# Kernel optimization log

Hardware: AMD Instinct MI355X
Metric: run time of the kernel (lower is better)

## Reference

```python
import jax, jax.numpy as jnp
import numpy as np


def setup_inputs() -> dict:
    key = jax.random.key(0)
    k1, k2, k3 = jax.random.split(key, 3)
    B, S, D = 4, 2048, 4096
    C, E = 8, 8  # num_clusters, experts per cluster
    hidden_states = jax.random.normal(k1, (B, S, D), dtype=jnp.float32)
    W_cluster = jax.random.normal(k2, (C, D), dtype=jnp.float32) * 0.02
    W_experts = jax.random.normal(k3, (C, E, D), dtype=jnp.float32) * 0.02
    expert_ids = jnp.arange(C * E, dtype=jnp.int64).reshape(C, E)
    return {"hidden_states": hidden_states, "W_cluster": W_cluster,
            "W_experts": W_experts, "expert_ids": expert_ids}


def reference(hidden_states, W_cluster, W_experts, expert_ids):
    # hidden_states: [B, S, D]; W_cluster: [C, D]; W_experts: [C, E, D]; expert_ids: [C, E]
    B, S, D = hidden_states.shape
    C, E, _ = W_experts.shape
    num_total = C * E
    x = hidden_states.reshape(-1, D)                      # [T, D]
    T = x.shape[0]
    # First-level: token-level top-1 cluster routing (cluster_token_routing=True).
    # softmax is monotone, so argmax over logits == argmax over softmax weights.
    cluster_logits = x @ W_cluster.T                      # [T, C]
    cluster_idx = jnp.argmax(cluster_logits, axis=-1)     # [T]
    # Second-level: expert logits for every cluster, then gather the chosen cluster's.
    all_logits = jnp.einsum('td,ced->tce', x, W_experts)  # [T, C, E]
    rows = jnp.arange(T)
    sel_logits = all_logits[rows, cluster_idx]            # [T, E]
    cols = expert_ids[cluster_idx]                        # [T, E] global expert slots
    neg_min = jnp.finfo(hidden_states.dtype).min
    routing = jnp.full((T, num_total), neg_min, dtype=hidden_states.dtype)
    routing = routing.at[rows[:, None], cols].set(sel_logits)
    return routing.reshape(B, S, num_total)
```

## Files before the change

kernel.cpp:

```cpp
#include <hip/hip_runtime.h>
#include <cfloat>

#define DDIM 4096
#define NCLUS 8
#define NEXP 8
#define NOUT 64
#define FILL_BITS 0xFF7F0000u

template <int M>
__device__ __forceinline__ void rs_step(float* a, int lane) {
#pragma unroll
  for (int i = 0; i < M; ++i) {
    float send = (lane & M) ? a[i] : a[i + M];
    float recv = __shfl_xor(send, M, 64);
    a[i] = ((lane & M) ? a[i + M] : a[i]) + recv;
  }
}

__device__ __forceinline__ void reduce32(float* a, int lane) {
#pragma unroll
  for (int i = 0; i < 32; ++i) a[i] += __shfl_xor(a[i], 32, 64);
  rs_step<16>(a, lane);
  rs_step<8>(a, lane);
  rs_step<4>(a, lane);
  rs_step<2>(a, lane);
  rs_step<1>(a, lane);
}

__global__ __launch_bounds__(256) void k_gate(const float* __restrict__ x,
                                              const float* __restrict__ Wc,
                                              const float* __restrict__ We,
                                              const int* __restrict__ eids32,
                                              float* __restrict__ out) {
  const int lane = threadIdx.x & 63;
  const int gw = blockIdx.x * 4 + (threadIdx.x >> 6);
  const int t0 = gw * 4;

  const float* xp = x + (size_t)t0 * DDIM + lane * 4;

  float a[32];
#pragma unroll
  for (int i = 0; i < 32; ++i) a[i] = 0.f;
  {
    const float* wp = Wc + lane * 4;
#pragma unroll 2
    for (int k = 0; k < 16; ++k) {
      const int base = k * 256;
      float4 xv[4];
#pragma unroll
      for (int t = 0; t < 4; ++t)
        xv[t] = *(const float4*)(xp + (size_t)t * DDIM + base);
#pragma unroll
      for (int c = 0; c < NCLUS; ++c) {
        const float4 w = *(const float4*)(wp + (size_t)c * DDIM + base);
#pragma unroll
        for (int t = 0; t < 4; ++t) {
          a[t * 8 + c] += xv[t].x * w.x;
          a[t * 8 + c] += xv[t].y * w.y;
          a[t * 8 + c] += xv[t].z * w.z;
          a[t * 8 + c] += xv[t].w * w.w;
        }
      }
    }
  }
  reduce32(a, lane);

  float v = a[0];
  int ci = lane & 7;
#pragma unroll
  for (int m = 1; m <= 4; m <<= 1) {
    float ov = __shfl_xor(v, m, 64);
    int oc = __shfl_xor(ci, m, 64);
    if (ov > v || (ov == v && oc < ci)) { v = ov; ci = oc; }
  }
  int c_of[4];
#pragma unroll
  for (int t = 0; t < 4; ++t)
    c_of[t] = __builtin_amdgcn_readfirstlane(__shfl(ci, 8 * t, 64));

  float b[32];
#pragma unroll
  for (int i = 0; i < 32; ++i) b[i] = 0.f;
  {
#pragma unroll 2
    for (int k = 0; k < 16; ++k) {
      const int base = k * 256;
      float4 xv[4];
#pragma unroll
      for (int t = 0; t < 4; ++t)
        xv[t] = *(const float4*)(xp + (size_t)t * DDIM + base);
#pragma unroll
      for (int c = 0; c < NCLUS; ++c) {
        if (c_of[0] == c || c_of[1] == c || c_of[2] == c || c_of[3] == c) {
          const float* wq = We + (size_t)c * NEXP * DDIM + lane * 4 + base;
          float4 wv[8];
#pragma unroll
          for (int e = 0; e < NEXP; ++e)
            wv[e] = *(const float4*)(wq + (size_t)e * DDIM);
#pragma unroll
          for (int t = 0; t < 4; ++t) {
            if (c_of[t] == c) {
#pragma unroll
              for (int e = 0; e < NEXP; ++e) {
                b[t * 8 + e] += xv[t].x * wv[e].x;
                b[t * 8 + e] += xv[t].y * wv[e].y;
                b[t * 8 + e] += xv[t].z * wv[e].z;
                b[t * 8 + e] += xv[t].w * wv[e].w;
              }
            }
          }
        }
      }
    }
  }
  reduce32(b, lane);
  const float vB = b[0];

  const int is64 = (eids32[1] == 0) ? 1 : 0;
  const float fillv = __uint_as_float(FILL_BITS);
#pragma unroll
  for (int t = 0; t < 4; ++t) {
    const int cc = c_of[t];
    float val = fillv;
#pragma unroll
    for (int e = 0; e < NEXP; ++e) {
      const float ve = __shfl(vB, 8 * t + e, 64);
      const int slot = cc * NEXP + e;
      const int col = is64 ? eids32[slot << 1] : eids32[slot];
      if (col == lane) val = ve;
    }
    out[(size_t)(t0 + t) * NOUT + lane] = val;
  }
}

extern "C" void kernel_launch(void* const* d_in, const int* in_sizes, int n_in,
                              void* d_out, int out_size, void* d_ws, size_t ws_size,
                              hipStream_t stream) {
  const float* x = (const float*)d_in[0];
  const float* Wc = (const float*)d_in[1];
  const float* We = (const float*)d_in[2];
  const int* eids = (const int*)d_in[3];
  float* out = (float*)d_out;

  const int T = in_sizes[0] / DDIM;
  k_gate<<<T / 16, 256, 0, stream>>>(x, Wc, We, eids, out);
}
```

Measured before the change: 248.3 us.

## Compute all gate logits with bf16 MFMA and split-K across waves

Replaces the scalar FP32 two-pass gating kernel with one MFMA pass. The pass computes cluster logits and all 64 expert logits together as a 16-token by 80-column tile, using bf16 16x16x32 MFMA with the K dimension split across 8 waves. Partial sums are reduced in shared memory, then argmax and scatter run from LDS. This drops the per-cluster branching and the FMA-bound inner loops, but it computes every expert logit rather than only the selected cluster's. Truncating to bf16 lowers accuracy and can flip argmax decisions on near-ties.

```diff
diff --git a/kernel.cpp b/kernel.cpp
--- a/kernel.cpp
+++ b/kernel.cpp
@@ -5,131 +5,102 @@
 #define NCLUS 8
 #define NEXP 8
 #define NOUT 64
+#define NW 72
+#define NCOL 80
 #define FILL_BITS 0xFF7F0000u
 
-template <int M>
-__device__ __forceinline__ void rs_step(float* a, int lane) {
-#pragma unroll
-  for (int i = 0; i < M; ++i) {
-    float send = (lane & M) ? a[i] : a[i + M];
-    float recv = __shfl_xor(send, M, 64);
-    a[i] = ((lane & M) ? a[i + M] : a[i]) + recv;
-  }
+typedef float floatx4 __attribute__((ext_vector_type(4)));
+typedef short bf16x8 __attribute__((ext_vector_type(8)));
+
+__device__ __forceinline__ short bfh(float f) {
+  return (short)(__float_as_uint(f) >> 16);
+}
+__device__ __forceinline__ bf16x8 pack8(const float4& a, const float4& b) {
+  bf16x8 r;
+  r[0] = bfh(a.x); r[1] = bfh(a.y); r[2] = bfh(a.z); r[3] = bfh(a.w);
+  r[4] = bfh(b.x); r[5] = bfh(b.y); r[6] = bfh(b.z); r[7] = bfh(b.w);
+  return r;
 }
 
-__device__ __forceinline__ void reduce32(float* a, int lane) {
+__global__ __launch_bounds__(512, 4) void k_mfma(const float* __restrict__ x,
+                                                 const float* __restrict__ Wc,
+                                                 const float* __restrict__ We,
+                                                 const int* __restrict__ eids32,
+                                                 float* __restrict__ out) {
+  __shared__ float s_acc[8][16 * NCOL];
+
+  const int tid = threadIdx.x;
+  const int lane = tid & 63;
+  const int wave = tid >> 6;
+  const int tile0 = blockIdx.x * 16;
+
+  const int m = lane & 15;
+  const int q = lane >> 4;
+  const int kw = wave * 512 + q * 8;
+
+  const float* xrow = x + (size_t)(tile0 + m) * DDIM + kw;
+
+  floatx4 acc[5];
 #pragma unroll
-  for (int i = 0; i < 32; ++i) a[i] += __shfl_xor(a[i], 32, 64);
-  rs_step<16>(a, lane);
-  rs_step<8>(a, lane);
-  rs_step<4>(a, lane);
-  rs_step<2>(a, lane);
-  rs_step<1>(a, lane);
-}
+  for (int ct = 0; ct < 5; ++ct) acc[ct] = (floatx4){0.f, 0.f, 0.f, 0.f};
 
-__global__ __launch_bounds__(256) void k_gate(const float* __restrict__ x,
-                                              const float* __restrict__ Wc,
-                                              const float* __restrict__ We,
-                                              const int* __restrict__ eids32,
-                                              float* __restrict__ out) {
-  const int lane = threadIdx.x & 63;
-  const int gw = blockIdx.x * 4 + (threadIdx.x >> 6);
-  const int t0 = gw * 4;
+#pragma unroll 2
+  for (int step = 0; step < 16; ++step) {
+    const int kb = step * 32;
+    const float4 a0 = *(const float4*)(xrow + kb);
+    const float4 a1 = *(const float4*)(xrow + kb + 4);
+    const bf16x8 af = pack8(a0, a1);
 
-  const float* xp = x + (size_t)t0 * DDIM + lane * 4;
-
-  float a[32];
 #pragma unroll
-  for (int i = 0; i < 32; ++i) a[i] = 0.f;
-  {
-    const float* wp = Wc + lane * 4;
-#pragma unroll 2
-    for (int k = 0; k < 16; ++k) {
-      const int base = k * 256;
-      float4 xv[4];
-#pragma unroll
-      for (int t = 0; t < 4; ++t)
-        xv[t] = *(const float4*)(xp + (size_t)t * DDIM + base);
-#pragma unroll
-      for (int c = 0; c < NCLUS; ++c) {
-        const float4 w = *(const float4*)(wp + (size_t)c * DDIM + base);
-#pragma unroll
-        for (int t = 0; t < 4; ++t) {
-          a[t * 8 + c] += xv[t].x * w.x;
-          a[t * 8 + c] += xv[t].y * w.y;
-          a[t * 8 + c] += xv[t].z * w.z;
-          a[t * 8 + c] += xv[t].w * w.w;
-        }
+    for (int ct = 0; ct < 5; ++ct) {
+      const int wrow = ct * 16 + m;
+      float4 b0 = {0.f, 0.f, 0.f, 0.f}, b1 = {0.f, 0.f, 0.f, 0.f};
+      if (wrow < NW) {
+        const float* bp = (wrow < NCLUS)
+                              ? (Wc + (size_t)wrow * DDIM)
+                              : (We + (size_t)(wrow - NCLUS) * DDIM);
+        b0 = *(const float4*)(bp + kw + kb);
+        b1 = *(const float4*)(bp + kw + kb + 4);
       }
+      const bf16x8 bf_ = pack8(b0, b1);
+      acc[ct] = __builtin_amdgcn_mfma_f32_16x16x32_bf16(af, bf_, acc[ct], 0, 0, 0);
     }
   }
-  reduce32(a, lane);
 
-  float v = a[0];
-  int ci = lane & 7;
 #pragma unroll
-  for (int m = 1; m <= 4; m <<= 1) {
-    float ov = __shfl_xor(v, m, 64);
-    int oc = __shfl_xor(ci, m, 64);
-    if (ov > v || (ov == v && oc < ci)) { v = ov; ci = oc; }
+  for (int ct = 0; ct < 5; ++ct)
+#pragma unroll
+    for (int r = 0; r < 4; ++r)
+      s_acc[wave][(q * 4 + r) * NCOL + ct * 16 + m] = acc[ct][r];
+  __syncthreads();
+
+  for (int i = tid; i < 16 * NCOL; i += 512) {
+    float s = s_acc[0][i];
+#pragma unroll
+    for (int w = 1; w < 8; ++w) s += s_acc[w][i];
+    s_acc[0][i] = s;
   }
-  int c_of[4];
-#pragma unroll
-  for (int t = 0; t < 4; ++t)
-    c_of[t] = __builtin_amdgcn_readfirstlane(__shfl(ci, 8 * t, 64));
-
-  float b[32];
-#pragma unroll
-  for (int i = 0; i < 32; ++i) b[i] = 0.f;
-  {
-#pragma unroll 2
-    for (int k = 0; k < 16; ++k) {
-      const int base = k * 256;
-      float4 xv[4];
-#pragma unroll
-      for (int t = 0; t < 4; ++t)
-        xv[t] = *(const float4*)(xp + (size_t)t * DDIM + base);
-#pragma unroll
-      for (int c = 0; c < NCLUS; ++c) {
-        if (c_of[0] == c || c_of[1] == c || c_of[2] == c || c_of[3] == c) {
-          const float* wq = We + (size_t)c * NEXP * DDIM + lane * 4 + base;
-          float4 wv[8];
-#pragma unroll
-          for (int e = 0; e < NEXP; ++e)
-            wv[e] = *(const float4*)(wq + (size_t)e * DDIM);
-#pragma unroll
-          for (int t = 0; t < 4; ++t) {
-            if (c_of[t] == c) {
-#pragma unroll
-              for (int e = 0; e < NEXP; ++e) {
-                b[t * 8 + e] += xv[t].x * wv[e].x;
-                b[t * 8 + e] += xv[t].y * wv[e].y;
-                b[t * 8 + e] += xv[t].z * wv[e].z;
-                b[t * 8 + e] += xv[t].w * wv[e].w;
-              }
-            }
-          }
-        }
-      }
-    }
-  }
-  reduce32(b, lane);
-  const float vB = b[0];
+  __syncthreads();
 
   const int is64 = (eids32[1] == 0) ? 1 : 0;
   const float fillv = __uint_as_float(FILL_BITS);
+  for (int idx = tid; idx < 16 * NOUT; idx += 512) {
+    const int tok = idx >> 6;
+    const int col = idx & 63;
+    const float* P = &s_acc[0][tok * NCOL];
+    float best = P[0];
+    int c = 0;
 #pragma unroll
-  for (int t = 0; t < 4; ++t) {
-    const int cc = c_of[t];
+    for (int cc = 1; cc < NCLUS; ++cc)
+      if (P[cc] > best) { best = P[cc]; c = cc; }
     float val = fillv;
 #pragma unroll
     for (int e = 0; e < NEXP; ++e) {
-      const float ve = __shfl(vB, 8 * t + e, 64);
-      const int slot = cc * NEXP + e;
-      const int col = is64 ? eids32[slot << 1] : eids32[slot];
-      if (col == lane) val = ve;
+      const int slot = c * NEXP + e;
+      const int ce = is64 ? eids32[slot << 1] : eids32[slot];
+      if (ce == col) val = P[NCLUS + slot];
     }
-    out[(size_t)(t0 + t) * NOUT + lane] = val;
+    out[(size_t)(tile0 + tok) * NOUT + col] = val;
   }
 }
 
@@ -143,5 +114,5 @@
   float* out = (float*)d_out;
 
   const int T = in_sizes[0] / DDIM;
-  k_gate<<<T / 16, 256, 0, stream>>>(x, Wc, We, eids, out);
+  k_mfma<<<T / 16, 512, 0, stream>>>(x, Wc, We, eids, out);
 }
```

After: 240.6 us. -3.1%, faster.
